# Kernel tuning notes

Measured on AMD Instinct MI355X. Metric: run time of the kernel, lower is better.

The kernel has to match this reference:

```python
import jax, jax.numpy as jnp
import numpy as np

B, N, D, H, K = 32, 100, 4, 256, 4  # batch, num_vars, input_size, n_hid, num_edge_types
SKIP_FIRST = True


def _edge_indices(n):
    e = np.ones((n, n)) - np.eye(n)
    s, r = np.where(e)
    return jnp.asarray(s, jnp.int32), jnp.asarray(r, jnp.int32)


def setup_inputs() -> dict:
    key = jax.random.key(0)
    ks = jax.random.split(key, 24)
    E = N * (N - 1)
    send, recv = _edge_indices(N)
    w = lambda k, shape: jax.random.normal(k, shape, jnp.float32) * 0.05
    b = lambda shape: jnp.full(shape, 0.1, jnp.float32)
    return {
        'inputs': jax.random.normal(ks[0], (B, N, D), jnp.float32),
        'hidden': jax.random.normal(ks[1], (B, N, H), jnp.float32),
        'edges': jax.random.uniform(ks[2], (B, E, K), jnp.float32),
        'msg_W1': w(ks[3], (K, 2 * H, H)), 'msg_b1': b((K, H)),
        'msg_W2': w(ks[4], (K, H, H)), 'msg_b2': b((K, H)),
        'Whr': w(ks[5], (H, H)), 'Whi': w(ks[6], (H, H)), 'Whh': w(ks[7], (H, H)),
        'Wir': w(ks[8], (D, H)), 'bir': b((H,)),
        'Wii': w(ks[9], (D, H)), 'bii': b((H,)),
        'Win': w(ks[10], (D, H)), 'bin_': b((H,)),
        'Wo1': w(ks[11], (H, H)), 'bo1': b((H,)),
        'Wo2': w(ks[12], (H, H)), 'bo2': b((H,)),
        'Wo3': w(ks[13], (H, D)), 'bo3': b((D,)),
        'send_edges': send, 'recv_edges': recv,
    }


def reference(inputs, hidden, edges, msg_W1, msg_b1, msg_W2, msg_b2,
              Whr, Whi, Whh, Wir, bir, Wii, bii, Win, bin_,
              Wo1, bo1, Wo2, bo2, Wo3, bo3, send_edges, recv_edges):
    # gather sender/receiver hidden states -> [B, E, 2H]
    pre_msg = jnp.concatenate([hidden[:, recv_edges], hidden[:, send_edges]], axis=-1)
    start = 1 if SKIP_FIRST else 0
    norm = float(K - 1) if SKIP_FIRST else float(K)
    all_msgs = jnp.zeros(pre_msg.shape[:2] + (H,), pre_msg.dtype)
    for i in range(start, K):  # fixed small loop over edge types
        m = jnp.tanh(pre_msg @ msg_W1[i] + msg_b1[i])
        m = jnp.tanh(m @ msg_W2[i] + msg_b2[i])
        all_msgs = all_msgs + m * edges[:, :, i:i + 1] / norm
    # scatter-sum messages to receiver nodes (== edge2node one-hot matmul)
    agg = jnp.zeros_like(hidden).at[:, recv_edges].add(all_msgs) / (N - 1)
    # GRU-style fused update
    r = jax.nn.sigmoid(inputs @ Wir + bir + agg @ Whr)
    i_g = jax.nn.sigmoid(inputs @ Wii + bii + agg @ Whi)
    n = jnp.tanh(inputs @ Win + bin_ + r * (agg @ Whh))
    hidden_new = (1.0 - i_g) * n + i_g * hidden
    # output MLP with residual (dropout p=0 in eval)
    pred = jax.nn.relu(hidden_new @ Wo1 + bo1)
    pred = jax.nn.relu(pred @ Wo2 + bo2)
    pred = inputs + (pred @ Wo3 + bo3)
    return pred, hidden_new
```

## Files before the change

### kernel.cpp

```cpp
#include <hip/hip_runtime.h>
#include <hip/hip_bf16.h>


typedef __attribute__((ext_vector_type(4))) float f32x4;
typedef __attribute__((ext_vector_type(8))) short s16x8;
typedef __attribute__((ext_vector_type(4))) unsigned short u16x4;
typedef __attribute__((ext_vector_type(4))) unsigned int u32x4;
typedef __attribute__((ext_vector_type(2))) unsigned int u32x2;

#define DEV static __device__ __forceinline__

DEV unsigned short f2bf(float f) {
  unsigned int u = __builtin_bit_cast(unsigned int, f);
  u += 0x7fffu + ((u >> 16) & 1u);
  return (unsigned short)(u >> 16);
}
DEV float bf2f(unsigned short h) {
  unsigned int u = ((unsigned int)h) << 16;
  return __builtin_bit_cast(float, u);
}
DEV float bflo(unsigned int u) { return __builtin_bit_cast(float, u << 16); }
DEV float bfhi(unsigned int u) { return __builtin_bit_cast(float, u & 0xffff0000u); }
DEV float exp2_fast(float x) { return __builtin_amdgcn_exp2f(x); }
DEV float tanh_fast(float x) {
  float e = exp2_fast(x * 2.885390082f);
  return 1.f - 2.f * __builtin_amdgcn_rcpf(e + 1.f);
}
DEV float sigmoid_fast(float x) {
  return __builtin_amdgcn_rcpf(1.f + exp2_fast(-1.442695041f * x));
}
DEV unsigned int pk_fp8x4(float a, float b, float c, float d) {
  int v = __builtin_amdgcn_cvt_pk_fp8_f32(a, b, 0, false);
  v = __builtin_amdgcn_cvt_pk_fp8_f32(c, d, v, true);
  return (unsigned int)v;
}

DEV void stage_bf16_64(const unsigned short* __restrict__ src, unsigned char* smem, int tid) {
#pragma unroll
  for (int j = 0; j < 8; ++j) {
    int c = tid + 256 * j;
    int s = c >> 5, hc = c & 31;
    s16x8 v = *reinterpret_cast<const s16x8*>(src + s * 256 + hc * 8);
    int byte = (s * 512 + hc * 16) ^ ((s & 7) << 4);
    *reinterpret_cast<s16x8*>(smem + byte) = v;
  }
}
DEV void stage_f32_64(const float* __restrict__ src, unsigned char* smem, int tid) {
#pragma unroll
  for (int j = 0; j < 8; ++j) {
    int c = tid + 256 * j;
    int s = c >> 5, hc = c & 31;
    const float* p = src + s * 256 + hc * 8;
    f32x4 v0 = *reinterpret_cast<const f32x4*>(p);
    f32x4 v1 = *reinterpret_cast<const f32x4*>(p + 4);
    s16x8 o;
#pragma unroll
    for (int i = 0; i < 4; ++i) { o[i] = (short)f2bf(v0[i]); o[4 + i] = (short)f2bf(v1[i]); }
    int byte = (s * 512 + hc * 16) ^ ((s & 7) << 4);
    *reinterpret_cast<s16x8*>(smem + byte) = o;
  }
}
DEV void stage_sum3_f32(const float* __restrict__ sa, const float* __restrict__ sb,
                        const float* __restrict__ sc, unsigned char* smem, int tid) {
#pragma unroll
  for (int j = 0; j < 8; ++j) {
    int c = tid + 256 * j;
    int s = c >> 5, hc = c & 31;
    int o4 = s * 256 + hc * 8;
    f32x4 a0 = *reinterpret_cast<const f32x4*>(sa + o4);
    f32x4 a1 = *reinterpret_cast<const f32x4*>(sa + o4 + 4);
    f32x4 b0 = *reinterpret_cast<const f32x4*>(sb + o4);
    f32x4 b1 = *reinterpret_cast<const f32x4*>(sb + o4 + 4);
    f32x4 c0 = *reinterpret_cast<const f32x4*>(sc + o4);
    f32x4 c1 = *reinterpret_cast<const f32x4*>(sc + o4 + 4);
    s16x8 o;
#pragma unroll
    for (int i = 0; i < 4; ++i) {
      o[i] = (short)f2bf(a0[i] + b0[i] + c0[i]);
      o[4 + i] = (short)f2bf(a1[i] + b1[i] + c1[i]);
    }
    int byte = (s * 512 + hc * 16) ^ ((s & 7) << 4);
    *reinterpret_cast<s16x8*>(smem + byte) = o;
  }
}

template<int MF>
DEV void gemm_lds_tile(const unsigned char* smemA, const unsigned short* __restrict__ B,
                       int nb, int lane, f32x4 acc[][4]) {
  int li = lane & 15, lg = lane >> 4;
#pragma unroll
  for (int kk = 0; kk < 8; ++kk) {
    int kb = kk * 32 + lg * 8;
    s16x8 a[MF];
#pragma unroll
    for (int m = 0; m < MF; ++m) {
      int row = m * 16 + li;
      int byte = (row * 512 + kb * 2) ^ ((row & 7) << 4);
      a[m] = *reinterpret_cast<const s16x8*>(smemA + byte);
    }
#pragma unroll
    for (int n = 0; n < 4; ++n) {
      int col = nb + n * 16 + li;
      s16x8 bf = *reinterpret_cast<const s16x8*>(B + col * 256 + kb);
#pragma unroll
      for (int m = 0; m < MF; ++m)
        acc[m][n] = __builtin_amdgcn_mfma_f32_16x16x32_bf16(a[m], bf, acc[m][n], 0, 0, 0);
    }
  }
}

__global__ __launch_bounds__(256) void k0_pack(
    const float* __restrict__ msg_W1,
    const float* __restrict__ Whr, const float* __restrict__ Whi, const float* __restrict__ Whh,
    const float* __restrict__ Wo1, const float* __restrict__ Wo2,
    unsigned short* __restrict__ W1aT, unsigned short* __restrict__ W1bT,
    unsigned short* __restrict__ WhT) {
  int g = blockIdx.x * 256 + threadIdx.x;
  if (g < 196608) {
    int ti = g >> 16, rem = g & 65535, n = rem >> 8, k = rem & 255;
    W1aT[g] = f2bf(msg_W1[((ti + 1) * 512 + k) * 256 + n]);
  } else if (g < 393216) {
    int h = g - 196608; int ti = h >> 16, rem = h & 65535, n = rem >> 8, k = rem & 255;
    W1bT[h] = f2bf(msg_W1[((ti + 1) * 512 + 256 + k) * 256 + n]);
  } else if (g < 720896) {
    int h = g - 393216; int mi = h >> 16, rem = h & 65535, n = rem >> 8, k = rem & 255;
    const float* s = mi == 0 ? Whr : mi == 1 ? Whi : mi == 2 ? Whh : mi == 3 ? Wo1 : Wo2;
    WhT[h] = f2bf(s[k * 256 + n]);
  }
}

__global__ __launch_bounds__(256) void k0_quant(
    const float* __restrict__ msg_W2, unsigned short* __restrict__ W2Q) {
  int g = blockIdx.x * 256 + threadIdx.x;
  int ti = g >> 15, rem = g & 32767, col = rem >> 7, k2 = rem & 127;
  int k = k2 * 2;
  const float* src = msg_W2 + (size_t)(ti + 1) * 65536;
  float a = src[k * 256 + col], b = src[(k + 1) * 256 + col];
  int v = __builtin_amdgcn_cvt_pk_fp8_f32(a, b, 0, false);
  W2Q[g] = (unsigned short)(v & 0xffff);
}

__global__ __launch_bounds__(256) void k_xpre(
    const float* __restrict__ inputs, const float* __restrict__ Wir, const float* __restrict__ bir,
    const float* __restrict__ Wii, const float* __restrict__ bii,
    const float* __restrict__ Win, const float* __restrict__ bin_, float* __restrict__ Xpre) {
  int g = blockIdx.x * 256 + threadIdx.x;
  int row = g / 768, c = g % 768, which = c >> 8, col = c & 255;
  const float* W = which == 0 ? Wir : which == 1 ? Wii : Win;
  const float* bb = which == 0 ? bir : which == 1 ? bii : bin_;
  const float* inp = inputs + row * 4;
  float s = bb[col];
#pragma unroll
  for (int d = 0; d < 4; ++d) s += inp[d] * W[d * 256 + col];
  Xpre[g] = s;
}

__global__ __launch_bounds__(256) void k1_nodepre(
    const float* __restrict__ hidden, const float* __restrict__ msg_b1,
    const unsigned short* __restrict__ W1aT, const unsigned short* __restrict__ W1bT,
    unsigned short* __restrict__ Ha, unsigned short* __restrict__ Hb) {
  __shared__ alignas(16) unsigned char smem[32768];
  int tid = threadIdx.x, lane = tid & 63, wv = tid >> 6;
  int mt = blockIdx.x, g = blockIdx.y;
  stage_f32_64(hidden + (size_t)mt * 64 * 256, smem, tid);
  __syncthreads();
  int ti = g < 3 ? g : g - 3;
  const unsigned short* Bp = (g < 3 ? W1aT : W1bT) + ti * 65536;
  f32x4 zz = {0.f, 0.f, 0.f, 0.f};
  f32x4 acc[4][4];
#pragma unroll
  for (int m = 0; m < 4; ++m)
#pragma unroll
    for (int n = 0; n < 4; ++n) acc[m][n] = zz;
  gemm_lds_tile<4>(smem, Bp, wv * 64, lane, acc);
  unsigned short* dst = (g < 3 ? Ha : Hb) + (size_t)ti * 819200 + (size_t)mt * 64 * 256;
  int li = lane & 15, lg = lane >> 4;
#pragma unroll
  for (int n = 0; n < 4; ++n) {
    int col = wv * 64 + n * 16 + li;
    float bias = g < 3 ? msg_b1[(ti + 1) * 256 + col] : 0.f;
#pragma unroll
    for (int m = 0; m < 4; ++m)
#pragma unroll
      for (int q = 0; q < 4; ++q) {
        int row = m * 16 + lg * 4 + q;
        dst[row * 256 + col] = f2bf(acc[m][n][q] + bias);
      }
  }
}

__global__ __launch_bounds__(256) void k2a_build(
    const unsigned short* __restrict__ Ha, const unsigned short* __restrict__ Hb,
    unsigned char* __restrict__ m1G, int ti) {
  int tid = threadIdx.x;
  int bid0 = blockIdx.x;
  int bid = (bid0 & 7) * 400 + (bid0 >> 3);
  int b = bid / 100, r = bid % 100;
  int hc = tid & 31, srow0 = tid >> 5;

  u32x4 hau = *reinterpret_cast<const u32x4*>(
      Ha + ((size_t)ti * 3200 + b * 100 + r) * 256 + hc * 8);
  float ha_f[8];
#pragma unroll
  for (int i = 0; i < 4; ++i) { ha_f[2 * i] = bflo(hau[i]); ha_f[2 * i + 1] = bfhi(hau[i]); }
  const unsigned short* HbB = Hb + ((size_t)ti * 3200 + b * 100) * 256;
  unsigned char* dst = m1G + (size_t)bid * 28672;
#pragma unroll
  for (int j = 0; j < 14; ++j) {
    int s = srow0 + 8 * j;
    u32x2 o = {0u, 0u};
    if (s < 99) {
      int snode = s + (s >= r ? 1 : 0);
      u32x4 hb = *reinterpret_cast<const u32x4*>(HbB + snode * 256 + hc * 8);
      float t[8];
#pragma unroll
      for (int i = 0; i < 4; ++i) {
        t[2 * i] = tanh_fast(ha_f[2 * i] + bflo(hb[i]));
        t[2 * i + 1] = tanh_fast(ha_f[2 * i + 1] + bfhi(hb[i]));
      }
      o[0] = pk_fp8x4(t[0], t[1], t[2], t[3]);
      o[1] = pk_fp8x4(t[4], t[5], t[6], t[7]);
    }
    *reinterpret_cast<u32x2*>(dst + s * 256 + hc * 8) = o;
  }
}

__global__ __launch_bounds__(256) void k2b_gemm(
    const float* __restrict__ edges, const float* __restrict__ msg_b2,
    const unsigned char* __restrict__ m1G, const unsigned char* __restrict__ W2Q,
    float* __restrict__ pagg, int ti) {
  __shared__ alignas(16) unsigned char smem[30144];
  float* w_s = (float*)(smem + 28672);
  float* agg_s = (float*)(smem + 29120);
  int tid = threadIdx.x, lane = tid & 63, wv = tid >> 6;
  int li = lane & 15, lg = lane >> 4;
  int bid0 = blockIdx.x;
  int bid = (bid0 & 7) * 400 + (bid0 >> 3);
  int b = bid / 100, r = bid % 100;

  if (tid < 112) {
    float w0 = 0.f;
    if (tid < 99) {
      int snode = tid + (tid >= r ? 1 : 0);
      int e = snode * 99 + r - (r > snode ? 1 : 0);
      w0 = edges[(size_t)(b * 9900 + e) * 4 + (ti + 1)] * (1.f / 297.f);
    }
    w_s[tid] = w0;
  }
  const unsigned char* src = m1G + (size_t)bid * 28672;
#pragma unroll
  for (int jj = 0; jj < 7; ++jj) {
    int idx = tid + 256 * jj;
    int s = idx >> 4, c16 = (idx & 15) * 16;
    u32x4 v = *reinterpret_cast<const u32x4*>(src + s * 256 + c16);
    int byte = (s * 256 + c16) ^ ((s & 7) << 4);
    *reinterpret_cast<u32x4*>(smem + byte) = v;
  }
  __syncthreads();

  float b2r[4];
#pragma unroll
  for (int n = 0; n < 4; ++n)
    b2r[n] = msg_b2[(ti + 1) * 256 + wv * 64 + n * 16 + li];

  float aggacc[4] = {0.f, 0.f, 0.f, 0.f};
  f32x4 zz = {0.f, 0.f, 0.f, 0.f};
  const unsigned char* Bq = W2Q + (size_t)ti * 65536;
#pragma unroll
  for (int p = 0; p < 2; ++p) {
    f32x4 acc[7][2];
#pragma unroll
    for (int m = 0; m < 7; ++m) { acc[m][0] = zz; acc[m][1] = zz; }
#pragma unroll
    for (int kk = 0; kk < 8; ++kk) {
      int ko = kk * 32 + lg * 8;
      long a[7];
#pragma unroll
      for (int m = 0; m < 7; ++m) {
        int row = m * 16 + li;
        int byte = (row * 256 + ko) ^ ((row & 7) << 4);
        a[m] = *reinterpret_cast<const long*>(smem + byte);
      }
#pragma unroll
      for (int n = 0; n < 2; ++n) {
        int col = wv * 64 + p * 32 + n * 16 + li;
        long bq = *reinterpret_cast<const long*>(Bq + col * 256 + ko);
#pragma unroll
        for (int m = 0; m < 7; ++m)
          acc[m][n] = __builtin_amdgcn_mfma_f32_16x16x32_fp8_fp8(a[m], bq, acc[m][n], 0, 0, 0);
      }
    }
#pragma unroll
    for (int n = 0; n < 2; ++n) {
      float b2v = b2r[p * 2 + n];
      float pa = 0.f;
#pragma unroll
      for (int m = 0; m < 7; ++m) {
        f32x4 wf = *reinterpret_cast<const f32x4*>(w_s + m * 16 + lg * 4);
#pragma unroll
        for (int q = 0; q < 4; ++q)
          pa += tanh_fast(acc[m][n][q] + b2v) * wf[q];
      }
      aggacc[p * 2 + n] += pa;
    }
  }

#pragma unroll
  for (int n = 0; n < 4; ++n) {
    float v = aggacc[n];
    v += __shfl_xor(v, 16);
    v += __shfl_xor(v, 32);
    if (lane < 16) agg_s[wv * 64 + n * 16 + lane] = v;
  }
  __syncthreads();
  pagg[(size_t)ti * 819200 + (size_t)bid * 256 + tid] = agg_s[tid];
}

__global__ __launch_bounds__(256) void k3_gemm(
    const float* __restrict__ pagg, const unsigned short* __restrict__ WhT,
    float* __restrict__ RIH) {
  __shared__ alignas(16) unsigned char smem[32768];
  int tid = threadIdx.x, lane = tid & 63, wv = tid >> 6;
  int mt = blockIdx.x, y = blockIdx.y;
  size_t base = (size_t)mt * 64 * 256;
  stage_sum3_f32(pagg + base, pagg + 819200 + base, pagg + 1638400 + base, smem, tid);
  __syncthreads();
  f32x4 zz = {0.f, 0.f, 0.f, 0.f};
  f32x4 acc[4][4];
#pragma unroll
  for (int m = 0; m < 4; ++m)
#pragma unroll
    for (int n = 0; n < 4; ++n) acc[m][n] = zz;
  gemm_lds_tile<4>(smem, WhT + y * 65536, wv * 64, lane, acc);
  float* dst = RIH + (size_t)y * 819200 + base;
  int li = lane & 15, lg = lane >> 4;
#pragma unroll
  for (int n = 0; n < 4; ++n) {
    int col = wv * 64 + n * 16 + li;
#pragma unroll
    for (int m = 0; m < 4; ++m)
#pragma unroll
      for (int q = 0; q < 4; ++q)
        dst[(m * 16 + lg * 4 + q) * 256 + col] = acc[m][n][q];
  }
}

__global__ __launch_bounds__(256) void k4_gru(
    const float* __restrict__ Xpre, const float* __restrict__ RIH,
    const float* __restrict__ hidden, float* __restrict__ out, unsigned short* __restrict__ hnewbf) {
  int idx = blockIdx.x * 256 + threadIdx.x;
  int row = idx >> 8, col = idx & 255;
  float xr = Xpre[row * 768 + col];
  float xi = Xpre[row * 768 + 256 + col];
  float xn = Xpre[row * 768 + 512 + col];
  float rr = sigmoid_fast(xr + RIH[idx]);
  float ig = sigmoid_fast(xi + RIH[819200 + idx]);
  float nn = tanh_fast(xn + rr * RIH[1638400 + idx]);
  float hn = (1.f - ig) * nn + ig * hidden[idx];
  out[12800 + idx] = hn;
  hnewbf[idx] = f2bf(hn);
}

__global__ __launch_bounds__(256) void k_mlp(
    const unsigned short* __restrict__ A, const unsigned short* __restrict__ WT,
    const float* __restrict__ bias, unsigned short* __restrict__ dst) {
  __shared__ alignas(16) unsigned char smem[32768];
  int tid = threadIdx.x, lane = tid & 63, wv = tid >> 6;
  int mt = blockIdx.x;
  stage_bf16_64(A + (size_t)mt * 64 * 256, smem, tid);
  __syncthreads();
  f32x4 zz = {0.f, 0.f, 0.f, 0.f};
  f32x4 acc[4][4];
#pragma unroll
  for (int m = 0; m < 4; ++m)
#pragma unroll
    for (int n = 0; n < 4; ++n) acc[m][n] = zz;
  gemm_lds_tile<4>(smem, WT, wv * 64, lane, acc);
  unsigned short* d = dst + (size_t)mt * 64 * 256;
  int li = lane & 15, lg = lane >> 4;
#pragma unroll
  for (int n = 0; n < 4; ++n) {
    int col = wv * 64 + n * 16 + li;
    float bv = bias[col];
#pragma unroll
    for (int m = 0; m < 4; ++m)
#pragma unroll
      for (int q = 0; q < 4; ++q) {
        float v = fmaxf(acc[m][n][q] + bv, 0.f);
        d[(m * 16 + lg * 4 + q) * 256 + col] = f2bf(v);
      }
  }
}

__global__ __launch_bounds__(64) void k7_out(
    const unsigned short* __restrict__ pred2, const float* __restrict__ Wo3,
    const float* __restrict__ bo3, const float* __restrict__ inputs, float* __restrict__ out) {
  int row = blockIdx.x, lane = threadIdx.x;
  u16x4 p = *reinterpret_cast<const u16x4*>(pred2 + (size_t)row * 256 + lane * 4);
  float s0 = 0.f, s1 = 0.f, s2 = 0.f, s3 = 0.f;
#pragma unroll
  for (int j = 0; j < 4; ++j) {
    float pv = bf2f(p[j]);
    const float* wr = Wo3 + (lane * 4 + j) * 4;
    s0 += pv * wr[0]; s1 += pv * wr[1]; s2 += pv * wr[2]; s3 += pv * wr[3];
  }
#pragma unroll
  for (int off = 32; off >= 1; off >>= 1) {
    s0 += __shfl_xor(s0, off); s1 += __shfl_xor(s1, off);
    s2 += __shfl_xor(s2, off); s3 += __shfl_xor(s3, off);
  }
  if (lane == 0) {
    out[row * 4 + 0] = inputs[row * 4 + 0] + s0 + bo3[0];
    out[row * 4 + 1] = inputs[row * 4 + 1] + s1 + bo3[1];
    out[row * 4 + 2] = inputs[row * 4 + 2] + s2 + bo3[2];
    out[row * 4 + 3] = inputs[row * 4 + 3] + s3 + bo3[3];
  }
}

extern "C" void kernel_launch(void* const* d_in, const int* in_sizes, int n_in,
                              void* d_out, int out_size, void* d_ws, size_t ws_size,
                              hipStream_t stream) {
  const float* inputs = (const float*)d_in[0];
  const float* hidden = (const float*)d_in[1];
  const float* edges  = (const float*)d_in[2];
  const float* msg_W1 = (const float*)d_in[3];
  const float* msg_b1 = (const float*)d_in[4];
  const float* msg_W2 = (const float*)d_in[5];
  const float* msg_b2 = (const float*)d_in[6];
  const float* Whr = (const float*)d_in[7];
  const float* Whi = (const float*)d_in[8];
  const float* Whh = (const float*)d_in[9];
  const float* Wir = (const float*)d_in[10];
  const float* bir = (const float*)d_in[11];
  const float* Wii = (const float*)d_in[12];
  const float* bii = (const float*)d_in[13];
  const float* Win = (const float*)d_in[14];
  const float* bin_ = (const float*)d_in[15];
  const float* Wo1 = (const float*)d_in[16];
  const float* bo1 = (const float*)d_in[17];
  const float* Wo2 = (const float*)d_in[18];
  const float* bo2 = (const float*)d_in[19];
  const float* Wo3 = (const float*)d_in[20];
  const float* bo3 = (const float*)d_in[21];
  float* out = (float*)d_out;

  char* ws = (char*)d_ws;
  size_t off = 0;
  auto take = [&](size_t bytes) -> char* {
    char* p = ws + off;
    off += (bytes + 511) & ~(size_t)511;
    return p;
  };
  unsigned short* W1aT = (unsigned short*)take(196608 * 2);
  unsigned short* W1bT = (unsigned short*)take(196608 * 2);
  unsigned short* W2Q  = (unsigned short*)take(196608);
  unsigned short* WhT  = (unsigned short*)take(327680 * 2);
  unsigned short* Ha   = (unsigned short*)take(2457600 * 2);
  unsigned short* Hb   = (unsigned short*)take(2457600 * 2);
  float* pagg = (float*)take(3 * 819200 * 4);
  unsigned char* m1G = (unsigned char*)take((size_t)3200 * 28672);
  float* Xpre = (float*)take(2457600 * 4);
  float* RIH  = (float*)take(2457600 * 4);
  unsigned short* hnewbf = (unsigned short*)take(819200 * 2);
  unsigned short* pred1  = (unsigned short*)take(819200 * 2);
  unsigned short* pred2  = (unsigned short*)take(819200 * 2);

  k0_pack<<<2816, 256, 0, stream>>>(msg_W1, Whr, Whi, Whh, Wo1, Wo2, W1aT, W1bT, WhT);
  k0_quant<<<384, 256, 0, stream>>>(msg_W2, W2Q);
  k_xpre<<<9600, 256, 0, stream>>>(inputs, Wir, bir, Wii, bii, Win, bin_, Xpre);
  k1_nodepre<<<dim3(50, 6), 256, 0, stream>>>(hidden, msg_b1, W1aT, W1bT, Ha, Hb);
  for (int ti = 0; ti < 3; ++ti) {
    k2a_build<<<3200, 256, 0, stream>>>(Ha, Hb, m1G, ti);
    k2b_gemm<<<3200, 256, 0, stream>>>(edges, msg_b2, m1G,
                                       (const unsigned char*)W2Q, pagg, ti);
  }
  k3_gemm<<<dim3(50, 3), 256, 0, stream>>>(pagg, WhT, RIH);
  k4_gru<<<3200, 256, 0, stream>>>(Xpre, RIH, hidden, out, hnewbf);
  k_mlp<<<50, 256, 0, stream>>>(hnewbf, WhT + 196608, bo1, pred1);
  k_mlp<<<50, 256, 0, stream>>>(pred1, WhT + 262144, bo2, pred2);
  k7_out<<<3200, 64, 0, stream>>>(pred2, Wo3, bo3, inputs, out);
}
```

Measured before the change: 354.2 us.

## Split k2b message GEMM rows across two blocks per receiver

Each k2b block previously processed all 112 (padded) sender rows for one receiver. The work is now split along a new grid dimension: one block handles rows 0-63 and the other rows 64-111. Each block writes its own partial aggregate, and k3 sums six partial buffers instead of three. This halves per-block LDS use and doubles the block count to raise occupancy and shorten the tail, at the cost of reloading W2 fragments twice, duplicating the edge-weight loads, and adding extra partial-sum traffic.

Result: slower. 490.8 us (+38.6%).

```diff
diff --git a/kernel.cpp b/kernel.cpp
--- a/kernel.cpp
+++ b/kernel.cpp
@@ -60,25 +60,22 @@
     *reinterpret_cast<s16x8*>(smem + byte) = o;
   }
 }
-DEV void stage_sum3_f32(const float* __restrict__ sa, const float* __restrict__ sb,
-                        const float* __restrict__ sc, unsigned char* smem, int tid) {
+DEV void stage_sum6_f32(const float* __restrict__ pagg, size_t base,
+                        unsigned char* smem, int tid) {
 #pragma unroll
   for (int j = 0; j < 8; ++j) {
     int c = tid + 256 * j;
     int s = c >> 5, hc = c & 31;
-    int o4 = s * 256 + hc * 8;
-    f32x4 a0 = *reinterpret_cast<const f32x4*>(sa + o4);
-    f32x4 a1 = *reinterpret_cast<const f32x4*>(sa + o4 + 4);
-    f32x4 b0 = *reinterpret_cast<const f32x4*>(sb + o4);
-    f32x4 b1 = *reinterpret_cast<const f32x4*>(sb + o4 + 4);
-    f32x4 c0 = *reinterpret_cast<const f32x4*>(sc + o4);
-    f32x4 c1 = *reinterpret_cast<const f32x4*>(sc + o4 + 4);
+    size_t o4 = base + s * 256 + hc * 8;
+    f32x4 a0 = {0.f, 0.f, 0.f, 0.f}, a1 = {0.f, 0.f, 0.f, 0.f};
+#pragma unroll
+    for (int k = 0; k < 6; ++k) {
+      a0 += *reinterpret_cast<const f32x4*>(pagg + (size_t)k * 819200 + o4);
+      a1 += *reinterpret_cast<const f32x4*>(pagg + (size_t)k * 819200 + o4 + 4);
+    }
     s16x8 o;
 #pragma unroll
-    for (int i = 0; i < 4; ++i) {
-      o[i] = (short)f2bf(a0[i] + b0[i] + c0[i]);
-      o[4 + i] = (short)f2bf(a1[i] + b1[i] + c1[i]);
-    }
+    for (int i = 0; i < 4; ++i) { o[i] = (short)f2bf(a0[i]); o[4 + i] = (short)f2bf(a1[i]); }
     int byte = (s * 512 + hc * 16) ^ ((s & 7) << 4);
     *reinterpret_cast<s16x8*>(smem + byte) = o;
   }
@@ -225,17 +222,78 @@
   }
 }
 
+template<int MF, int RB>
+DEV void k2b_body(const unsigned char* __restrict__ src,
+                  const unsigned char* __restrict__ Bq,
+                  const float* __restrict__ msg_b2, int ti,
+                  unsigned char* smem, const float* w_s,
+                  int tid, float aggacc[4]) {
+  int lane = tid & 63, wv = tid >> 6;
+  int li = lane & 15, lg = lane >> 4;
+#pragma unroll
+  for (int j = 0; j < MF; ++j) {
+    int idx = tid + 256 * j;
+    int sl = idx >> 4, c16 = (idx & 15) * 16;
+    u32x4 v = *reinterpret_cast<const u32x4*>(src + (RB + sl) * 256 + c16);
+    int byte = (sl * 256 + c16) ^ ((sl & 7) << 4);
+    *reinterpret_cast<u32x4*>(smem + byte) = v;
+  }
+  __syncthreads();
+
+  f32x4 zz = {0.f, 0.f, 0.f, 0.f};
+#pragma unroll
+  for (int p = 0; p < 2; ++p) {
+    f32x4 acc[MF][2];
+#pragma unroll
+    for (int m = 0; m < MF; ++m) { acc[m][0] = zz; acc[m][1] = zz; }
+#pragma unroll
+    for (int kk = 0; kk < 8; ++kk) {
+      int ko = kk * 32 + lg * 8;
+      long a[MF];
+#pragma unroll
+      for (int m = 0; m < MF; ++m) {
+        int lr = m * 16 + li;
+        int byte = (lr * 256 + ko) ^ ((lr & 7) << 4);
+        a[m] = *reinterpret_cast<const long*>(smem + byte);
+      }
+#pragma unroll
+      for (int n = 0; n < 2; ++n) {
+        int col = wv * 64 + p * 32 + n * 16 + li;
+        long bq = *reinterpret_cast<const long*>(Bq + col * 256 + ko);
+#pragma unroll
+        for (int m = 0; m < MF; ++m)
+          acc[m][n] = __builtin_amdgcn_mfma_f32_16x16x32_fp8_fp8(a[m], bq, acc[m][n], 0, 0, 0);
+      }
+    }
+    f32x4 wf[MF];
+#pragma unroll
+    for (int m = 0; m < MF; ++m)
+      wf[m] = *reinterpret_cast<const f32x4*>(w_s + RB + m * 16 + lg * 4);
+#pragma unroll
+    for (int n = 0; n < 2; ++n) {
+      float b2v = msg_b2[(ti + 1) * 256 + wv * 64 + p * 32 + n * 16 + li];
+      float pa = 0.f;
+#pragma unroll
+      for (int m = 0; m < MF; ++m)
+#pragma unroll
+        for (int q = 0; q < 4; ++q)
+          pa += tanh_fast(acc[m][n][q] + b2v) * wf[m][q];
+      aggacc[p * 2 + n] += pa;
+    }
+  }
+}
+
 __global__ __launch_bounds__(256) void k2b_gemm(
     const float* __restrict__ edges, const float* __restrict__ msg_b2,
     const unsigned char* __restrict__ m1G, const unsigned char* __restrict__ W2Q,
     float* __restrict__ pagg, int ti) {
-  __shared__ alignas(16) unsigned char smem[30144];
-  float* w_s = (float*)(smem + 28672);
-  float* agg_s = (float*)(smem + 29120);
+  __shared__ alignas(16) unsigned char smem[17856];
+  float* w_s = (float*)(smem + 16384);
+  float* agg_s = (float*)(smem + 16832);
   int tid = threadIdx.x, lane = tid & 63, wv = tid >> 6;
-  int li = lane & 15, lg = lane >> 4;
   int bid0 = blockIdx.x;
   int bid = (bid0 & 7) * 400 + (bid0 >> 3);
+  int g = blockIdx.y;
   int b = bid / 100, r = bid % 100;
 
   if (tid < 112) {
@@ -247,63 +305,14 @@
     }
     w_s[tid] = w0;
   }
+
+  float aggacc[4] = {0.f, 0.f, 0.f, 0.f};
   const unsigned char* src = m1G + (size_t)bid * 28672;
-#pragma unroll
-  for (int jj = 0; jj < 7; ++jj) {
-    int idx = tid + 256 * jj;
-    int s = idx >> 4, c16 = (idx & 15) * 16;
-    u32x4 v = *reinterpret_cast<const u32x4*>(src + s * 256 + c16);
-    int byte = (s * 256 + c16) ^ ((s & 7) << 4);
-    *reinterpret_cast<u32x4*>(smem + byte) = v;
-  }
-  __syncthreads();
-
-  float b2r[4];
-#pragma unroll
-  for (int n = 0; n < 4; ++n)
-    b2r[n] = msg_b2[(ti + 1) * 256 + wv * 64 + n * 16 + li];
-
-  float aggacc[4] = {0.f, 0.f, 0.f, 0.f};
-  f32x4 zz = {0.f, 0.f, 0.f, 0.f};
   const unsigned char* Bq = W2Q + (size_t)ti * 65536;
-#pragma unroll
-  for (int p = 0; p < 2; ++p) {
-    f32x4 acc[7][2];
-#pragma unroll
-    for (int m = 0; m < 7; ++m) { acc[m][0] = zz; acc[m][1] = zz; }
-#pragma unroll
-    for (int kk = 0; kk < 8; ++kk) {
-      int ko = kk * 32 + lg * 8;
-      long a[7];
-#pragma unroll
-      for (int m = 0; m < 7; ++m) {
-        int row = m * 16 + li;
-        int byte = (row * 256 + ko) ^ ((row & 7) << 4);
-        a[m] = *reinterpret_cast<const long*>(smem + byte);
-      }
-#pragma unroll
-      for (int n = 0; n < 2; ++n) {
-        int col = wv * 64 + p * 32 + n * 16 + li;
-        long bq = *reinterpret_cast<const long*>(Bq + col * 256 + ko);
-#pragma unroll
-        for (int m = 0; m < 7; ++m)
-          acc[m][n] = __builtin_amdgcn_mfma_f32_16x16x32_fp8_fp8(a[m], bq, acc[m][n], 0, 0, 0);
-      }
-    }
-#pragma unroll
-    for (int n = 0; n < 2; ++n) {
-      float b2v = b2r[p * 2 + n];
-      float pa = 0.f;
-#pragma unroll
-      for (int m = 0; m < 7; ++m) {
-        f32x4 wf = *reinterpret_cast<const f32x4*>(w_s + m * 16 + lg * 4);
-#pragma unroll
-        for (int q = 0; q < 4; ++q)
-          pa += tanh_fast(acc[m][n][q] + b2v) * wf[q];
-      }
-      aggacc[p * 2 + n] += pa;
-    }
-  }
+  if (g == 0)
+    k2b_body<4, 0>(src, Bq, msg_b2, ti, smem, w_s, tid, aggacc);
+  else
+    k2b_body<3, 64>(src, Bq, msg_b2, ti, smem, w_s, tid, aggacc);
 
 #pragma unroll
   for (int n = 0; n < 4; ++n) {
@@ -313,7 +322,7 @@
     if (lane < 16) agg_s[wv * 64 + n * 16 + lane] = v;
   }
   __syncthreads();
-  pagg[(size_t)ti * 819200 + (size_t)bid * 256 + tid] = agg_s[tid];
+  pagg[((size_t)(ti * 2 + g) * 3200 + bid) * 256 + tid] = agg_s[tid];
 }
 
 __global__ __launch_bounds__(256) void k3_gemm(
@@ -323,7 +332,7 @@
   int tid = threadIdx.x, lane = tid & 63, wv = tid >> 6;
   int mt = blockIdx.x, y = blockIdx.y;
   size_t base = (size_t)mt * 64 * 256;
-  stage_sum3_f32(pagg + base, pagg + 819200 + base, pagg + 1638400 + base, smem, tid);
+  stage_sum6_f32(pagg, base, smem, tid);
   __syncthreads();
   f32x4 zz = {0.f, 0.f, 0.f, 0.f};
   f32x4 acc[4][4];
@@ -457,7 +466,7 @@
   unsigned short* WhT  = (unsigned short*)take(327680 * 2);
   unsigned short* Ha   = (unsigned short*)take(2457600 * 2);
   unsigned short* Hb   = (unsigned short*)take(2457600 * 2);
-  float* pagg = (float*)take(3 * 819200 * 4);
+  float* pagg = (float*)take((size_t)6 * 819200 * 4);
   unsigned char* m1G = (unsigned char*)take((size_t)3200 * 28672);
   float* Xpre = (float*)take(2457600 * 4);
   float* RIH  = (float*)take(2457600 * 4);
@@ -471,8 +480,8 @@
   k1_nodepre<<<dim3(50, 6), 256, 0, stream>>>(hidden, msg_b1, W1aT, W1bT, Ha, Hb);
   for (int ti = 0; ti < 3; ++ti) {
     k2a_build<<<3200, 256, 0, stream>>>(Ha, Hb, m1G, ti);
-    k2b_gemm<<<3200, 256, 0, stream>>>(edges, msg_b2, m1G,
-                                       (const unsigned char*)W2Q, pagg, ti);
+    k2b_gemm<<<dim3(3200, 2), 256, 0, stream>>>(edges, msg_b2, m1G,
+                                                (const unsigned char*)W2Q, pagg, ti);
   }
   k3_gemm<<<dim3(50, 3), 256, 0, stream>>>(pagg, WhT, RIH);
   k4_gru<<<3200, 256, 0, stream>>>(Xpre, RIH, hidden, out, hnewbf);
```

## Process two tiles per k2b block with register-prefetched double buffering

Applied to the files above, without the earlier changes.

Each k2b_gemm block now handles two (batch, receiver) tiles instead of one, and the grid is halved. The second tile's message data and edge weights are loaded into registers while the first tile's MFMA GEMM runs, then written into a second LDS buffer. This hides global-load latency behind compute, at the cost of doubled LDS per block (about 60 KB), which lowers occupancy, and more live registers.

After: 462.6 us. +30.6%, slower.

```diff
diff --git a/kernel.cpp b/kernel.cpp
--- a/kernel.cpp
+++ b/kernel.cpp
@@ -225,95 +225,149 @@
   }
 }
 
+DEV float k2b_loadw(const float* __restrict__ edges, int b, int r, int ti, int tid) {
+  float w0 = 0.f;
+  if (tid < 99) {
+    int snode = tid + (tid >= r ? 1 : 0);
+    int e = snode * 99 + r - (r > snode ? 1 : 0);
+    w0 = edges[(size_t)(b * 9900 + e) * 4 + (ti + 1)] * (1.f / 297.f);
+  }
+  return w0;
+}
+DEV void k2b_compute(const unsigned char* __restrict__ buf,
+                     const unsigned char* __restrict__ Bq,
+                     const float* __restrict__ w_s, const float b2r[4],
+                     float* __restrict__ agg_dst, int tid) {
+  int lane = tid & 63, wv = tid >> 6;
+  int li = lane & 15, lg = lane >> 4;
+  f32x4 zz = {0.f, 0.f, 0.f, 0.f};
+  float aggacc[4] = {0.f, 0.f, 0.f, 0.f};
+#pragma unroll
+  for (int p = 0; p < 2; ++p) {
+    f32x4 acc[7][2];
+#pragma unroll
+    for (int m = 0; m < 7; ++m) { acc[m][0] = zz; acc[m][1] = zz; }
+#pragma unroll
+    for (int kk = 0; kk < 8; ++kk) {
+      int ko = kk * 32 + lg * 8;
+      long a[7];
+#pragma unroll
+      for (int m = 0; m < 7; ++m) {
+        int row = m * 16 + li;
+        int byte = (row * 256 + ko) ^ ((row & 7) << 4);
+        a[m] = *reinterpret_cast<const long*>(buf + byte);
+      }
+#pragma unroll
+      for (int n = 0; n < 2; ++n) {
+        int col = wv * 64 + p * 32 + n * 16 + li;
+        long bq = *reinterpret_cast<const long*>(Bq + col * 256 + ko);
+#pragma unroll
+        for (int m = 0; m < 7; ++m)
+          acc[m][n] = __builtin_amdgcn_mfma_f32_16x16x32_fp8_fp8(a[m], bq, acc[m][n], 0, 0, 0);
+      }
+    }
+#pragma unroll
+    for (int n = 0; n < 2; ++n) {
+      float b2v = b2r[p * 2 + n];
+      float pa = 0.f;
+#pragma unroll
+      for (int m = 0; m < 7; ++m) {
+        f32x4 wf = *reinterpret_cast<const f32x4*>(w_s + m * 16 + lg * 4);
+#pragma unroll
+        for (int q = 0; q < 4; ++q)
+          pa += tanh_fast(acc[m][n][q] + b2v) * wf[q];
+      }
+      aggacc[p * 2 + n] += pa;
+    }
+  }
+#pragma unroll
+  for (int n = 0; n < 4; ++n) {
+    float v = aggacc[n];
+    v += __shfl_xor(v, 16);
+    v += __shfl_xor(v, 32);
+    if (lane < 16) agg_dst[wv * 64 + n * 16 + lane] = v;
+  }
+}
+
 __global__ __launch_bounds__(256) void k2b_gemm(
     const float* __restrict__ edges, const float* __restrict__ msg_b2,
     const unsigned char* __restrict__ m1G, const unsigned char* __restrict__ W2Q,
     float* __restrict__ pagg, int ti) {
-  __shared__ alignas(16) unsigned char smem[30144];
-  float* w_s = (float*)(smem + 28672);
-  float* agg_s = (float*)(smem + 29120);
+  __shared__ alignas(16) unsigned char smem[60288];
+  float* w_s = (float*)(smem + 57344);
+  float* agg_s = (float*)(smem + 58240);
   int tid = threadIdx.x, lane = tid & 63, wv = tid >> 6;
-  int li = lane & 15, lg = lane >> 4;
+  int li = lane & 15;
   int bid0 = blockIdx.x;
-  int bid = (bid0 & 7) * 400 + (bid0 >> 3);
-  int b = bid / 100, r = bid % 100;
-
-  if (tid < 112) {
-    float w0 = 0.f;
-    if (tid < 99) {
-      int snode = tid + (tid >= r ? 1 : 0);
-      int e = snode * 99 + r - (r > snode ? 1 : 0);
-      w0 = edges[(size_t)(b * 9900 + e) * 4 + (ti + 1)] * (1.f / 297.f);
-    }
-    w_s[tid] = w0;
-  }
-  const unsigned char* src = m1G + (size_t)bid * 28672;
-#pragma unroll
-  for (int jj = 0; jj < 7; ++jj) {
-    int idx = tid + 256 * jj;
-    int s = idx >> 4, c16 = (idx & 15) * 16;
-    u32x4 v = *reinterpret_cast<const u32x4*>(src + s * 256 + c16);
-    int byte = (s * 256 + c16) ^ ((s & 7) << 4);
-    *reinterpret_cast<u32x4*>(smem + byte) = v;
-  }
-  __syncthreads();
+  int bid = (bid0 & 7) * 200 + (bid0 >> 3);
+  int tile0 = bid, tile1 = bid + 1600;
+  int b0 = tile0 / 100, r0 = tile0 % 100;
+  int b1 = tile1 / 100, r1 = tile1 % 100;
 
   float b2r[4];
 #pragma unroll
   for (int n = 0; n < 4; ++n)
     b2r[n] = msg_b2[(ti + 1) * 256 + wv * 64 + n * 16 + li];
 
-  float aggacc[4] = {0.f, 0.f, 0.f, 0.f};
-  f32x4 zz = {0.f, 0.f, 0.f, 0.f};
+  int sRow = tid >> 4, c16 = (tid & 15) * 16;
+
+  {
+    const unsigned char* src = m1G + (size_t)tile0 * 28672;
+    float w0 = k2b_loadw(edges, b0, r0, ti, tid);
+#pragma unroll
+    for (int j = 0; j < 7; ++j) {
+      int idx = tid + 256 * j;
+      u32x4 v = *reinterpret_cast<const u32x4*>(src + (size_t)idx * 16);
+      int row = sRow + 16 * j;
+      int byte = (row * 256 + c16) ^ ((row & 7) << 4);
+      *reinterpret_cast<u32x4*>(smem + byte) = v;
+    }
+    if (tid < 112) w_s[tid] = w0;
+  }
+  __syncthreads();
+
   const unsigned char* Bq = W2Q + (size_t)ti * 65536;
-#pragma unroll
-  for (int p = 0; p < 2; ++p) {
-    f32x4 acc[7][2];
-#pragma unroll
-    for (int m = 0; m < 7; ++m) { acc[m][0] = zz; acc[m][1] = zz; }
-#pragma unroll
-    for (int kk = 0; kk < 8; ++kk) {
-      int ko = kk * 32 + lg * 8;
-      long a[7];
-#pragma unroll
-      for (int m = 0; m < 7; ++m) {
-        int row = m * 16 + li;
-        int byte = (row * 256 + ko) ^ ((row & 7) << 4);
-        a[m] = *reinterpret_cast<const long*>(smem + byte);
-      }
-#pragma unroll
-      for (int n = 0; n < 2; ++n) {
-        int col = wv * 64 + p * 32 + n * 16 + li;
-        long bq = *reinterpret_cast<const long*>(Bq + col * 256 + ko);
-#pragma unroll
-        for (int m = 0; m < 7; ++m)
-          acc[m][n] = __builtin_amdgcn_mfma_f32_16x16x32_fp8_fp8(a[m], bq, acc[m][n], 0, 0, 0);
-      }
-    }
-#pragma unroll
-    for (int n = 0; n < 2; ++n) {
-      float b2v = b2r[p * 2 + n];
-      float pa = 0.f;
-#pragma unroll
-      for (int m = 0; m < 7; ++m) {
-        f32x4 wf = *reinterpret_cast<const f32x4*>(w_s + m * 16 + lg * 4);
-#pragma unroll
-        for (int q = 0; q < 4; ++q)
-          pa += tanh_fast(acc[m][n][q] + b2v) * wf[q];
-      }
-      aggacc[p * 2 + n] += pa;
-    }
-  }
-
-#pragma unroll
-  for (int n = 0; n < 4; ++n) {
-    float v = aggacc[n];
-    v += __shfl_xor(v, 16);
-    v += __shfl_xor(v, 32);
-    if (lane < 16) agg_s[wv * 64 + n * 16 + lane] = v;
-  }
-  __syncthreads();
-  pagg[(size_t)ti * 819200 + (size_t)bid * 256 + tid] = agg_s[tid];
+
+  {
+    const unsigned char* src1 = m1G + (size_t)tile1 * 28672;
+    u32x4 v0 = *reinterpret_cast<const u32x4*>(src1 + (size_t)(tid + 0) * 16);
+    u32x4 v1 = *reinterpret_cast<const u32x4*>(src1 + (size_t)(tid + 256) * 16);
+    u32x4 v2 = *reinterpret_cast<const u32x4*>(src1 + (size_t)(tid + 512) * 16);
+    u32x4 v3 = *reinterpret_cast<const u32x4*>(src1 + (size_t)(tid + 768) * 16);
+    u32x4 v4 = *reinterpret_cast<const u32x4*>(src1 + (size_t)(tid + 1024) * 16);
+    u32x4 v5 = *reinterpret_cast<const u32x4*>(src1 + (size_t)(tid + 1280) * 16);
+    u32x4 v6 = *reinterpret_cast<const u32x4*>(src1 + (size_t)(tid + 1536) * 16);
+    float w1 = k2b_loadw(edges, b1, r1, ti, tid);
+
+    k2b_compute(smem, Bq, w_s, b2r, agg_s, tid);
+
+    unsigned char* buf1 = smem + 28672;
+    {
+      int row = sRow;          int byte = (row * 256 + c16) ^ ((row & 7) << 4);
+      *reinterpret_cast<u32x4*>(buf1 + byte) = v0;
+    }
+    { int row = sRow + 16;  int byte = (row * 256 + c16) ^ ((row & 7) << 4);
+      *reinterpret_cast<u32x4*>(buf1 + byte) = v1; }
+    { int row = sRow + 32;  int byte = (row * 256 + c16) ^ ((row & 7) << 4);
+      *reinterpret_cast<u32x4*>(buf1 + byte) = v2; }
+    { int row = sRow + 48;  int byte = (row * 256 + c16) ^ ((row & 7) << 4);
+      *reinterpret_cast<u32x4*>(buf1 + byte) = v3; }
+    { int row = sRow + 64;  int byte = (row * 256 + c16) ^ ((row & 7) << 4);
+      *reinterpret_cast<u32x4*>(buf1 + byte) = v4; }
+    { int row = sRow + 80;  int byte = (row * 256 + c16) ^ ((row & 7) << 4);
+      *reinterpret_cast<u32x4*>(buf1 + byte) = v5; }
+    { int row = sRow + 96;  int byte = (row * 256 + c16) ^ ((row & 7) << 4);
+      *reinterpret_cast<u32x4*>(buf1 + byte) = v6; }
+    if (tid < 112) w_s[112 + tid] = w1;
+    __syncthreads();
+    pagg[(size_t)ti * 819200 + (size_t)tile0 * 256 + tid] = agg_s[tid];
+  }
+
+  {
+    k2b_compute(smem + 28672, Bq, w_s + 112, b2r, agg_s + 256, tid);
+    __syncthreads();
+    pagg[(size_t)ti * 819200 + (size_t)tile1 * 256 + tid] = agg_s[256 + tid];
+  }
 }
 
 __global__ __launch_bounds__(256) void k3_gemm(
@@ -471,7 +525,7 @@
   k1_nodepre<<<dim3(50, 6), 256, 0, stream>>>(hidden, msg_b1, W1aT, W1bT, Ha, Hb);
   for (int ti = 0; ti < 3; ++ti) {
     k2a_build<<<3200, 256, 0, stream>>>(Ha, Hb, m1G, ti);
-    k2b_gemm<<<3200, 256, 0, stream>>>(edges, msg_b2, m1G,
+    k2b_gemm<<<1600, 256, 0, stream>>>(edges, msg_b2, m1G,
                                        (const unsigned char*)W2Q, pagg, ti);
   }
   k3_gemm<<<dim3(50, 3), 256, 0, stream>>>(pagg, WhT, RIH);
```

## Software-pipeline edge-type build and GEMM kernels with double-buffered message tiles

Applied to the files above, without the earlier changes.

Splits the per-edge-type build and GEMM bodies into device functions and launches a combined kernel in which odd blocks build the fp8 message tile for the next edge type while even blocks run the GEMM for the current one. The single message buffer becomes two ping-pong buffers, so six launches become four. The goal is to overlap the memory-bound build phase with the compute-bound GEMM phase and cut launch gaps. In exchange, the fused kernel always reserves the GEMM's shared memory even for build blocks, and the extra buffer adds roughly 92MB of workspace.

Measured after the change: 402.9 us. +13.8%, slower.

```diff
diff --git a/kernel.cpp b/kernel.cpp
--- a/kernel.cpp
+++ b/kernel.cpp
@@ -189,12 +189,9 @@
   }
 }
 
-__global__ __launch_bounds__(256) void k2a_build(
-    const unsigned short* __restrict__ Ha, const unsigned short* __restrict__ Hb,
-    unsigned char* __restrict__ m1G, int ti) {
-  int tid = threadIdx.x;
-  int bid0 = blockIdx.x;
-  int bid = (bid0 & 7) * 400 + (bid0 >> 3);
+DEV void dev_build(const unsigned short* __restrict__ Ha, const unsigned short* __restrict__ Hb,
+                   unsigned char* __restrict__ m1G, int ti, int tileid, int tid) {
+  int bid = (tileid & 7) * 400 + (tileid >> 3);
   int b = bid / 100, r = bid % 100;
   int hc = tid & 31, srow0 = tid >> 5;
 
@@ -225,17 +222,15 @@
   }
 }
 
-__global__ __launch_bounds__(256) void k2b_gemm(
-    const float* __restrict__ edges, const float* __restrict__ msg_b2,
-    const unsigned char* __restrict__ m1G, const unsigned char* __restrict__ W2Q,
-    float* __restrict__ pagg, int ti) {
-  __shared__ alignas(16) unsigned char smem[30144];
+DEV void dev_gemm(const float* __restrict__ edges, const float* __restrict__ msg_b2,
+                  const unsigned char* __restrict__ m1G, const unsigned char* __restrict__ W2Q,
+                  float* __restrict__ pagg, int ti, int tileid, int tid,
+                  unsigned char* smem) {
   float* w_s = (float*)(smem + 28672);
   float* agg_s = (float*)(smem + 29120);
-  int tid = threadIdx.x, lane = tid & 63, wv = tid >> 6;
+  int lane = tid & 63, wv = tid >> 6;
   int li = lane & 15, lg = lane >> 4;
-  int bid0 = blockIdx.x;
-  int bid = (bid0 & 7) * 400 + (bid0 >> 3);
+  int bid = (tileid & 7) * 400 + (tileid >> 3);
   int b = bid / 100, r = bid % 100;
 
   if (tid < 112) {
@@ -314,6 +309,34 @@
   }
   __syncthreads();
   pagg[(size_t)ti * 819200 + (size_t)bid * 256 + tid] = agg_s[tid];
+}
+
+__global__ __launch_bounds__(256) void k2a_build(
+    const unsigned short* __restrict__ Ha, const unsigned short* __restrict__ Hb,
+    unsigned char* __restrict__ m1G, int ti) {
+  dev_build(Ha, Hb, m1G, ti, blockIdx.x, threadIdx.x);
+}
+
+__global__ __launch_bounds__(256) void k2b_gemm(
+    const float* __restrict__ edges, const float* __restrict__ msg_b2,
+    const unsigned char* __restrict__ m1G, const unsigned char* __restrict__ W2Q,
+    float* __restrict__ pagg, int ti) {
+  __shared__ alignas(16) unsigned char smem[30144];
+  dev_gemm(edges, msg_b2, m1G, W2Q, pagg, ti, blockIdx.x, threadIdx.x, smem);
+}
+
+__global__ __launch_bounds__(256) void k2ab_fused(
+    const unsigned short* __restrict__ Ha, const unsigned short* __restrict__ Hb,
+    const float* __restrict__ edges, const float* __restrict__ msg_b2,
+    unsigned char* __restrict__ m1Gb, const unsigned char* __restrict__ m1Gg,
+    const unsigned char* __restrict__ W2Q, float* __restrict__ pagg,
+    int ti_b, int ti_g) {
+  __shared__ alignas(16) unsigned char smem[30144];
+  int tileid = blockIdx.x >> 1;
+  if (blockIdx.x & 1)
+    dev_build(Ha, Hb, m1Gb, ti_b, tileid, threadIdx.x);
+  else
+    dev_gemm(edges, msg_b2, m1Gg, W2Q, pagg, ti_g, tileid, threadIdx.x, smem);
 }
 
 __global__ __launch_bounds__(256) void k3_gemm(
@@ -458,7 +481,8 @@
   unsigned short* Ha   = (unsigned short*)take(2457600 * 2);
   unsigned short* Hb   = (unsigned short*)take(2457600 * 2);
   float* pagg = (float*)take(3 * 819200 * 4);
-  unsigned char* m1G = (unsigned char*)take((size_t)3200 * 28672);
+  unsigned char* m1GA = (unsigned char*)take((size_t)3200 * 28672);
+  unsigned char* m1GB = (unsigned char*)take((size_t)3200 * 28672);
   float* Xpre = (float*)take(2457600 * 4);
   float* RIH  = (float*)take(2457600 * 4);
   unsigned short* hnewbf = (unsigned short*)take(819200 * 2);
@@ -469,11 +493,13 @@
   k0_quant<<<384, 256, 0, stream>>>(msg_W2, W2Q);
   k_xpre<<<9600, 256, 0, stream>>>(inputs, Wir, bir, Wii, bii, Win, bin_, Xpre);
   k1_nodepre<<<dim3(50, 6), 256, 0, stream>>>(hidden, msg_b1, W1aT, W1bT, Ha, Hb);
-  for (int ti = 0; ti < 3; ++ti) {
-    k2a_build<<<3200, 256, 0, stream>>>(Ha, Hb, m1G, ti);
-    k2b_gemm<<<3200, 256, 0, stream>>>(edges, msg_b2, m1G,
-                                       (const unsigned char*)W2Q, pagg, ti);
-  }
+  k2a_build<<<3200, 256, 0, stream>>>(Ha, Hb, m1GA, 0);
+  k2ab_fused<<<6400, 256, 0, stream>>>(Ha, Hb, edges, msg_b2, m1GB, m1GA,
+                                       (const unsigned char*)W2Q, pagg, 1, 0);
+  k2ab_fused<<<6400, 256, 0, stream>>>(Ha, Hb, edges, msg_b2, m1GA, m1GB,
+                                       (const unsigned char*)W2Q, pagg, 2, 1);
+  k2b_gemm<<<3200, 256, 0, stream>>>(edges, msg_b2, m1GA,
+                                     (const unsigned char*)W2Q, pagg, 2);
   k3_gemm<<<dim3(50, 3), 256, 0, stream>>>(pagg, WhT, RIH);
   k4_gru<<<3200, 256, 0, stream>>>(Xpre, RIH, hidden, out, hnewbf);
   k_mlp<<<50, 256, 0, stream>>>(hnewbf, WhT + 196608, bo1, pred1);
```
